# Kernel optimization log

Hardware: AMD Instinct MI355X
Metric: run time of the kernel (lower is better)

## Reference

```python
import jax, jax.numpy as jnp
import numpy as np

# ---- config (mirrors conf dict passed to RegionLoss.__init__) ----
ANCHORS = jnp.array([[1.3221, 1.73145], [3.19275, 4.00944], [5.05587, 8.09892],
                     [9.47112, 4.84053], [11.2364, 10.0071]], dtype=jnp.float32)
NUM_CLASSES = 80
OBJECT_SCALE = 5.0
NO_OBJECT_SCALE = 1.0
CLASS_SCALE = 1.0
COORD_SCALE = 1.0
SIL_THRESH = 0.6
SEEN = 0  # fresh module -> seen < 12800 warm-start branch is active


def _iou_center(a, b):
    """IoU of center-format boxes (cx, cy, w, h); a, b broadcastable [..., 4]."""
    ax1, ax2 = a[..., 0] - a[..., 2] * 0.5, a[..., 0] + a[..., 2] * 0.5
    ay1, ay2 = a[..., 1] - a[..., 3] * 0.5, a[..., 1] + a[..., 3] * 0.5
    bx1, bx2 = b[..., 0] - b[..., 2] * 0.5, b[..., 0] + b[..., 2] * 0.5
    by1, by2 = b[..., 1] - b[..., 3] * 0.5, b[..., 1] + b[..., 3] * 0.5
    iw = jnp.maximum(jnp.minimum(ax2, bx2) - jnp.maximum(ax1, bx1), 0.0)
    ih = jnp.maximum(jnp.minimum(ay2, by2) - jnp.maximum(ay1, by1), 0.0)
    inter = iw * ih
    union = a[..., 2] * a[..., 3] + b[..., 2] * b[..., 3] - inter
    return inter / union


def setup_inputs() -> dict:
    key = jax.random.key(0)
    k1, k2, k3, k4 = jax.random.split(key, 4)
    B, A, C, H, W, NBOX = 32, 5, NUM_CLASSES, 52, 52, 50
    pred = jax.random.normal(k1, (B, A * (C + 5), H, W), dtype=jnp.float32)
    cls = jax.random.randint(k2, (B, NBOX, 1), 0, C).astype(jnp.float32)
    xy = jax.random.uniform(k3, (B, NBOX, 2), minval=0.02, maxval=0.98, dtype=jnp.float32)
    wh = jax.random.uniform(k4, (B, NBOX, 2), minval=0.05, maxval=0.4, dtype=jnp.float32)
    target = jnp.concatenate([cls, xy, wh], axis=-1)  # (B, NBOX, 5): cls,x,y,w,h in [0,1]
    return {"pred": pred, "target": target, "train_out": 0}


def _region_loss(pred, target):
    B, H, W = pred.shape[0], pred.shape[2], pred.shape[3]
    A, C = ANCHORS.shape[0], NUM_CLASSES
    nbox = target.shape[1]
    p = pred.reshape(B, A, C + 5, H, W)

    txy = jax.nn.sigmoid(p[:, :, 0:2])                 # (B,A,2,H,W)
    twh = p[:, :, 2:4]                                 # (B,A,2,H,W)
    pred_no_off = jnp.concatenate([txy, twh], axis=2)  # (B,A,4,H,W)
    pred_conf = jax.nn.sigmoid(p[:, :, 4])             # (B,A,H,W)
    cls_logits = p[:, :, 5:]                           # (B,A,C,H,W)

    # decode boxes to grid units (detached in the original)
    grid_x = jnp.arange(W, dtype=p.dtype)              # broadcasts along W (last dim)
    grid_y = jnp.arange(H, dtype=p.dtype)[:, None]     # broadcasts along H
    aw = ANCHORS[:, 0][None, :, None, None]
    ah = ANCHORS[:, 1][None, :, None, None]
    bx = txy[:, :, 0] + grid_x
    by = txy[:, :, 1] + grid_y
    bw = jnp.exp(twh[:, :, 0]) * aw
    bh = jnp.exp(twh[:, :, 1]) * ah
    pred_boxes = jax.lax.stop_gradient(jnp.stack([bx, by, bw, bh], axis=-1))  # (B,A,H,W,4)

    # ground truth in grid units
    scale = jnp.array([W, H, W, H], dtype=p.dtype)
    gt = target[:, :, 1:5] * scale                     # (B,nbox,4) center format
    valid = target[:, :, 1] > 0                        # sentinel: x == 0 terminates

    # conf mask: zero-out cells whose best IoU vs any GT exceeds sil_thresh
    pb_flat = pred_boxes.reshape(B, A * H * W, 4)
    ious = _iou_center(gt[:, :, None, :], pb_flat[:, None, :, :])  # (B,nbox,A*H*W)
    ious = jnp.where(valid[:, :, None], ious, 0.0)
    max_iou = jnp.max(ious, axis=1).reshape(B, A, H, W)
    conf_mask = jnp.where(max_iou > SIL_THRESH, 0.0, NO_OBJECT_SCALE)

    # best anchor per GT via width/height-only IoU (boxes at origin)
    gw, gh = gt[..., 2], gt[..., 3]
    inter = jnp.minimum(gw[..., None], ANCHORS[:, 0]) * jnp.minimum(gh[..., None], ANCHORS[:, 1])
    union = gw[..., None] * gh[..., None] + ANCHORS[:, 0] * ANCHORS[:, 1] - inter
    best_a = jnp.argmax(inter / union, axis=-1)        # (B,nbox)

    gi = jnp.clip(gt[..., 0].astype(jnp.int32), 0, W - 1)
    gj = jnp.clip(gt[..., 1].astype(jnp.int32), 0, H - 1)
    b_idx = jnp.broadcast_to(jnp.arange(B)[:, None], (B, nbox))
    bi = jnp.where(valid, b_idx, B)                    # invalid GTs -> OOB batch, dropped

    aw_b = ANCHORS[best_a, 0]
    ah_b = ANCHORS[best_a, 1]
    tx_t = gt[..., 0] - gi.astype(p.dtype)
    ty_t = gt[..., 1] - gj.astype(p.dtype)
    tw_t = jnp.log(gw / aw_b)
    th_t = jnp.log(gh / ah_b)

    pred_box_at = pred_boxes[b_idx, best_a, gj, gi]    # (B,nbox,4) decoded box at GT cell
    iou_gt = _iou_center(gt, pred_box_at)              # (B,nbox)

    # initialize targets/masks (seen < 12800 warm start)
    if SEEN < 12800:
        coord_mask = jnp.ones((B, A, H, W), dtype=p.dtype)
        target_box = jnp.zeros((B, A, 4, H, W), dtype=p.dtype).at[:, :, 0:2].set(0.5)
    else:
        coord_mask = jnp.zeros((B, A, H, W), dtype=p.dtype)
        target_box = jnp.zeros((B, A, 4, H, W), dtype=p.dtype)
    cls_mask = jnp.zeros((B, A, H, W), dtype=p.dtype)
    target_conf = jnp.zeros((B, A, H, W), dtype=p.dtype)
    target_cls = jnp.zeros((B, A, H, W), dtype=p.dtype)

    coord_mask = coord_mask.at[bi, best_a, gj, gi].set(1.0, mode='drop')
    cls_mask = cls_mask.at[bi, best_a, gj, gi].set(1.0, mode='drop')
    conf_mask = conf_mask.at[bi, best_a, gj, gi].set(OBJECT_SCALE, mode='drop')
    target_box = target_box.at[bi, best_a, 0, gj, gi].set(tx_t, mode='drop')
    target_box = target_box.at[bi, best_a, 1, gj, gi].set(ty_t, mode='drop')
    target_box = target_box.at[bi, best_a, 2, gj, gi].set(tw_t, mode='drop')
    target_box = target_box.at[bi, best_a, 3, gj, gi].set(th_t, mode='drop')
    target_conf = target_conf.at[bi, best_a, gj, gi].set(iou_gt, mode='drop')
    target_cls = target_cls.at[bi, best_a, gj, gi].set(target[:, :, 0], mode='drop')

    # losses
    half = jnp.asarray(0.5, p.dtype)
    loss_x = COORD_SCALE * jnp.sum(((pred_no_off[:, :, 0] - target_box[:, :, 0]) * coord_mask) ** 2) * half
    loss_y = COORD_SCALE * jnp.sum(((pred_no_off[:, :, 1] - target_box[:, :, 1]) * coord_mask) ** 2) * half
    loss_w = COORD_SCALE * jnp.sum(((pred_no_off[:, :, 2] - target_box[:, :, 2]) * coord_mask) ** 2) * half
    loss_h = COORD_SCALE * jnp.sum(((pred_no_off[:, :, 3] - target_box[:, :, 3]) * coord_mask) ** 2) * half
    loss_conf = jnp.sum(((pred_conf - target_conf) * jnp.sqrt(conf_mask)) ** 2) * half

    logp = jax.nn.log_softmax(cls_logits, axis=2)      # (B,A,C,H,W)
    tcls = jnp.clip(target_cls.astype(jnp.int32), 0, C - 1)
    ce = -jnp.take_along_axis(logp, tcls[:, :, None], axis=2)[:, :, 0]  # (B,A,H,W)
    loss_cls = CLASS_SCALE * jnp.sum(cls_mask * ce)

    loss = loss_x + loss_y + loss_w + loss_h + loss_conf + loss_cls
    return loss, loss_x, loss_y, loss_w, loss_h, loss_conf, loss_cls


def reference(pred, target, train_out):
    out = _region_loss(pred, target)
    if train_out:
        return out
    return out[0]
```

## Files before the change

### kernel.cpp

```cpp
#include <hip/hip_runtime.h>
#include <math.h>

#define BB 32
#define AA 5
#define CC 80
#define HH 52
#define WW 52
#define NBOX 50
#define HWSZ (HH*WW)
#define CELLS (AA*HWSZ)

__constant__ float d_aw[AA] = {1.3221f, 3.19275f, 5.05587f, 9.47112f, 11.2364f};
__constant__ float d_ah[AA] = {1.73145f, 4.00944f, 8.09892f, 4.84053f, 10.0071f};

__device__ __forceinline__ float sig(float x) { return 1.f / (1.f + expf(-x)); }

__device__ __forceinline__ float wave_max(float v) {
    #pragma unroll
    for (int off = 32; off > 0; off >>= 1) v = fmaxf(v, __shfl_xor(v, off, 64));
    return v;
}
__device__ __forceinline__ float wave_sum(float v) {
    #pragma unroll
    for (int off = 32; off > 0; off >>= 1) v += __shfl_xor(v, off, 64);
    return v;
}

__global__ __launch_bounds__(256) void region_fused(const float* __restrict__ pred,
                                                    const float* __restrict__ target,
                                                    float* __restrict__ out) {
    __shared__ float4 s_box[NBOX];
    __shared__ float2 s_ac[NBOX];
    __shared__ float4 s_t[NBOX];
    __shared__ float2 s_m[NBOX];
    __shared__ float wsum[4];

    const int b = blockIdx.y;
    const int tid = threadIdx.x;
    const int lane = tid & 63;

    if (tid < NBOX) {
        const float* t = target + ((size_t)b * NBOX + tid) * 5;
        float t0 = t[0], t1 = t[1], t2 = t[2], t3 = t[3], t4 = t[4];
        float gx = t1 * (float)WW, gy = t2 * (float)HH;
        float gw = t3 * (float)WW, gh = t4 * (float)HH;
        bool valid = t1 > 0.f;
        int best = 0; float bestv = -1.f;
        #pragma unroll
        for (int a = 0; a < AA; ++a) {
            float inter = fminf(gw, d_aw[a]) * fminf(gh, d_ah[a]);
            float uni = gw * gh + d_aw[a] * d_ah[a] - inter;
            float r = inter / uni;
            if (r > bestv) { bestv = r; best = a; }
        }
        int gi = (int)gx; gi = gi < 0 ? 0 : (gi > WW - 1 ? WW - 1 : gi);
        int gj = (int)gy; gj = gj < 0 ? 0 : (gj > HH - 1 ? HH - 1 : gj);

        size_t bbase = ((size_t)(b * AA + best) * (CC + 5)) * HWSZ + (size_t)gj * WW + gi;
        float px = sig(pred[bbase]) + (float)gi;
        float py = sig(pred[bbase + HWSZ]) + (float)gj;
        float pw = expf(pred[bbase + 2 * HWSZ]) * d_aw[best];
        float ph = expf(pred[bbase + 3 * HWSZ]) * d_ah[best];

        float ax1 = gx - gw * 0.5f, ax2 = gx + gw * 0.5f;
        float ay1 = gy - gh * 0.5f, ay2 = gy + gh * 0.5f;
        float bx1 = px - pw * 0.5f, bx2 = px + pw * 0.5f;
        float by1 = py - ph * 0.5f, by2 = py + ph * 0.5f;
        float iw = fmaxf(fminf(ax2, bx2) - fmaxf(ax1, bx1), 0.f);
        float ih = fmaxf(fminf(ay2, by2) - fmaxf(ay1, by1), 0.f);
        float inter = iw * ih;
        float iou_gt = inter / (gw * gh + pw * ph - inter);

        if (valid) {
            s_box[tid] = make_float4(ax1, ax2, ay1, ay2);
            s_ac[tid]  = make_float2(0.375f * gw * gh,
                                     (float)(best * HWSZ + gj * WW + gi));
        } else {
            s_box[tid] = make_float4(0.f, 0.f, 0.f, 0.f);
            s_ac[tid]  = make_float2(0.f, -1.f);
        }
        s_t[tid] = make_float4(gx - (float)gi, gy - (float)gj,
                               logf(gw / d_aw[best]), logf(gh / d_ah[best]));
        s_m[tid] = make_float2(iou_gt, t0);
    }
    __syncthreads();

    const int c = blockIdx.x * 256 + tid;
    float lsum = 0.f;
    int win = -1;
    int a = 0, rem = 0, tcls = 0;
    if (c < CELLS) {
        a = c / HWSZ;
        rem = c - a * HWSZ;
        int hh = rem / WW;
        int wwi = rem - hh * WW;
        size_t base = ((size_t)(b * AA + a) * (CC + 5)) * HWSZ + rem;
        float p0 = pred[base];
        float p1 = pred[base + HWSZ];
        float p2 = pred[base + 2 * HWSZ];
        float p3 = pred[base + 3 * HWSZ];
        float p4 = pred[base + 4 * HWSZ];
        float tx = sig(p0);
        float ty = sig(p1);
        float conf = sig(p4);
        float bx = tx + (float)wwi;
        float by = ty + (float)hh;
        float bw = expf(p2) * d_aw[a];
        float bh = expf(p3) * d_ah[a];
        float px1 = bx - bw * 0.5f, px2 = bx + bw * 0.5f;
        float py1 = by - bh * 0.5f, py2 = by + bh * 0.5f;
        float tp = 0.375f * (bw * bh);
        float cf = (float)c;

        bool hit = false;
        #pragma unroll 5
        for (int j = 0; j < NBOX; ++j) {
            float4 r0 = s_box[j];
            float2 r1 = s_ac[j];
            float iw2 = fmaxf(fminf(px2, r0.y) - fmaxf(px1, r0.x), 0.f);
            float ih2 = fmaxf(fminf(py2, r0.w) - fmaxf(py1, r0.z), 0.f);
            float inter2 = iw2 * ih2;
            hit = hit | ((inter2 - tp) > r1.x);
            win = (r1.y == cf) ? j : win;
        }

        float dx, dy, dw, dh, lconf;
        if (win >= 0) {
            float4 r2 = s_t[win];
            float2 r3 = s_m[win];
            dx = tx - r2.x; dy = ty - r2.y; dw = p2 - r2.z; dh = p3 - r2.w;
            float d = conf - r3.x;
            lconf = 2.5f * d * d;
            int tc = (int)r3.y;
            tcls = tc < 0 ? 0 : (tc > CC - 1 ? CC - 1 : tc);
        } else {
            dx = tx - 0.5f; dy = ty - 0.5f; dw = p2; dh = p3;
            lconf = hit ? 0.f : 0.5f * conf * conf;
        }
        lsum = 0.5f * (dx * dx + dy * dy + dw * dw + dh * dh) + lconf;
    }

    unsigned long long mask = __ballot(win >= 0);
    while (mask) {
        int src = __ffsll(mask) - 1;
        mask &= mask - 1;
        int wa   = __shfl(a, src, 64);
        int wrem = __shfl(rem, src, 64);
        int wt   = __shfl(tcls, src, 64);
        size_t cbase = ((size_t)(b * AA + wa) * (CC + 5) + 5) * HWSZ + (size_t)wrem;
        float v1 = pred[cbase + (size_t)lane * HWSZ];
        float v2 = (lane < CC - 64) ? pred[cbase + (size_t)(lane + 64) * HWSZ]
                                    : -INFINITY;
        float mx = wave_max(fmaxf(v1, v2));
        float s = expf(v1 - mx) + ((lane < CC - 64) ? expf(v2 - mx) : 0.f);
        s = wave_sum(s);
        float vt = ((lane == wt) ? v1 : 0.f) + ((lane + 64 == wt) ? v2 : 0.f);
        vt = wave_sum(vt);
        if (lane == src) lsum += (mx + logf(s)) - vt;
    }

    #pragma unroll
    for (int off = 32; off > 0; off >>= 1)
        lsum += __shfl_down(lsum, off, 64);
    int wave = tid >> 6;
    if (lane == 0) wsum[wave] = lsum;
    __syncthreads();
    if (tid == 0) {
        atomicAdd(out, wsum[0] + wsum[1] + wsum[2] + wsum[3]);
    }
}

extern "C" void kernel_launch(void* const* d_in, const int* in_sizes, int n_in,
                              void* d_out, int out_size, void* d_ws, size_t ws_size,
                              hipStream_t stream) {
    const float* pred = (const float*)d_in[0];
    const float* target = (const float*)d_in[1];
    float* out = (float*)d_out;

    hipMemsetAsync(out, 0, sizeof(float) * out_size, stream);
    dim3 grid((CELLS + 255) / 256, BB);
    region_fused<<<grid, dim3(256), 0, stream>>>(pred, target, out);
}
```

Before: 204.7 us.

## Process four cells per thread to amortize per-block target setup and shared loads

Each thread now handles four grid cells strided by 16 blocks, and the grid shrinks from 53 to 16 blocks per batch image. The per-block target preprocessing and each shared-memory box read are reused across four cells in the inner IoU loop. This trades lower block count, and so less parallelism (512 blocks total), for less redundant setup work and more memory loads in flight per thread.

```diff
diff --git a/kernel.cpp b/kernel.cpp
--- a/kernel.cpp
+++ b/kernel.cpp
@@ -9,6 +9,8 @@
 #define NBOX 50
 #define HWSZ (HH*WW)
 #define CELLS (AA*HWSZ)
+#define NCH 4
+#define CSTRIDE (16*256)
 
 __constant__ float d_aw[AA] = {1.3221f, 3.19275f, 5.05587f, 9.47112f, 11.2364f};
 __constant__ float d_ah[AA] = {1.73145f, 4.00944f, 8.09892f, 4.84053f, 10.0071f};
@@ -85,21 +87,37 @@
     }
     __syncthreads();
 
-    const int c = blockIdx.x * 256 + tid;
+    const int c0 = blockIdx.x * 256 + tid;
+
+    float px1[NCH], px2[NCH], py1[NCH], py2[NCH], tp[NCH], cf[NCH];
+    float p2s[NCH], p3s[NCH], txs[NCH], tys[NCH], cfs[NCH];
+    int aA[NCH], remA[NCH], win[NCH], tcl[NCH];
+    bool hit[NCH], act[NCH];
+
     float lsum = 0.f;
-    int win = -1;
-    int a = 0, rem = 0, tcls = 0;
-    if (c < CELLS) {
-        a = c / HWSZ;
-        rem = c - a * HWSZ;
+
+    #pragma unroll
+    for (int k = 0; k < NCH; ++k) {
+        int c = c0 + k * CSTRIDE;
+        act[k] = (c < CELLS);
+        win[k] = -1;
+        hit[k] = false;
+        tcl[k] = 0;
+        int cc = act[k] ? c : 0;
+        int a = cc / HWSZ;
+        int rem = cc - a * HWSZ;
+        aA[k] = a; remA[k] = rem;
         int hh = rem / WW;
         int wwi = rem - hh * WW;
-        size_t base = ((size_t)(b * AA + a) * (CC + 5)) * HWSZ + rem;
-        float p0 = pred[base];
-        float p1 = pred[base + HWSZ];
-        float p2 = pred[base + 2 * HWSZ];
-        float p3 = pred[base + 3 * HWSZ];
-        float p4 = pred[base + 4 * HWSZ];
+        float p0 = 0.f, p1 = 0.f, p2 = 0.f, p3 = 0.f, p4 = 0.f;
+        if (act[k]) {
+            size_t base = ((size_t)(b * AA + a) * (CC + 5)) * HWSZ + rem;
+            p0 = pred[base];
+            p1 = pred[base + HWSZ];
+            p2 = pred[base + 2 * HWSZ];
+            p3 = pred[base + 3 * HWSZ];
+            p4 = pred[base + 4 * HWSZ];
+        }
         float tx = sig(p0);
         float ty = sig(p1);
         float conf = sig(p4);
@@ -107,56 +125,67 @@
         float by = ty + (float)hh;
         float bw = expf(p2) * d_aw[a];
         float bh = expf(p3) * d_ah[a];
-        float px1 = bx - bw * 0.5f, px2 = bx + bw * 0.5f;
-        float py1 = by - bh * 0.5f, py2 = by + bh * 0.5f;
-        float tp = 0.375f * (bw * bh);
-        float cf = (float)c;
-
-        bool hit = false;
-        #pragma unroll 5
-        for (int j = 0; j < NBOX; ++j) {
-            float4 r0 = s_box[j];
-            float2 r1 = s_ac[j];
-            float iw2 = fmaxf(fminf(px2, r0.y) - fmaxf(px1, r0.x), 0.f);
-            float ih2 = fmaxf(fminf(py2, r0.w) - fmaxf(py1, r0.z), 0.f);
+        px1[k] = bx - bw * 0.5f; px2[k] = bx + bw * 0.5f;
+        py1[k] = by - bh * 0.5f; py2[k] = by + bh * 0.5f;
+        tp[k] = 0.375f * (bw * bh);
+        cf[k] = act[k] ? (float)c : -2.f;
+        p2s[k] = p2; p3s[k] = p3; txs[k] = tx; tys[k] = ty; cfs[k] = conf;
+    }
+
+    #pragma unroll 2
+    for (int j = 0; j < NBOX; ++j) {
+        float4 r0 = s_box[j];
+        float2 r1 = s_ac[j];
+        #pragma unroll
+        for (int k = 0; k < NCH; ++k) {
+            float iw2 = fmaxf(fminf(px2[k], r0.y) - fmaxf(px1[k], r0.x), 0.f);
+            float ih2 = fmaxf(fminf(py2[k], r0.w) - fmaxf(py1[k], r0.z), 0.f);
             float inter2 = iw2 * ih2;
-            hit = hit | ((inter2 - tp) > r1.x);
-            win = (r1.y == cf) ? j : win;
-        }
-
+            hit[k] = hit[k] | ((inter2 - tp[k]) > r1.x);
+            win[k] = (r1.y == cf[k]) ? j : win[k];
+        }
+    }
+
+    #pragma unroll
+    for (int k = 0; k < NCH; ++k) {
+        if (!act[k]) continue;
+        float tx = txs[k], ty = tys[k], p2 = p2s[k], p3 = p3s[k], conf = cfs[k];
         float dx, dy, dw, dh, lconf;
-        if (win >= 0) {
-            float4 r2 = s_t[win];
-            float2 r3 = s_m[win];
+        if (win[k] >= 0) {
+            float4 r2 = s_t[win[k]];
+            float2 r3 = s_m[win[k]];
             dx = tx - r2.x; dy = ty - r2.y; dw = p2 - r2.z; dh = p3 - r2.w;
             float d = conf - r3.x;
             lconf = 2.5f * d * d;
             int tc = (int)r3.y;
-            tcls = tc < 0 ? 0 : (tc > CC - 1 ? CC - 1 : tc);
+            tcl[k] = tc < 0 ? 0 : (tc > CC - 1 ? CC - 1 : tc);
         } else {
             dx = tx - 0.5f; dy = ty - 0.5f; dw = p2; dh = p3;
-            lconf = hit ? 0.f : 0.5f * conf * conf;
-        }
-        lsum = 0.5f * (dx * dx + dy * dy + dw * dw + dh * dh) + lconf;
-    }
-
-    unsigned long long mask = __ballot(win >= 0);
-    while (mask) {
-        int src = __ffsll(mask) - 1;
-        mask &= mask - 1;
-        int wa   = __shfl(a, src, 64);
-        int wrem = __shfl(rem, src, 64);
-        int wt   = __shfl(tcls, src, 64);
-        size_t cbase = ((size_t)(b * AA + wa) * (CC + 5) + 5) * HWSZ + (size_t)wrem;
-        float v1 = pred[cbase + (size_t)lane * HWSZ];
-        float v2 = (lane < CC - 64) ? pred[cbase + (size_t)(lane + 64) * HWSZ]
-                                    : -INFINITY;
-        float mx = wave_max(fmaxf(v1, v2));
-        float s = expf(v1 - mx) + ((lane < CC - 64) ? expf(v2 - mx) : 0.f);
-        s = wave_sum(s);
-        float vt = ((lane == wt) ? v1 : 0.f) + ((lane + 64 == wt) ? v2 : 0.f);
-        vt = wave_sum(vt);
-        if (lane == src) lsum += (mx + logf(s)) - vt;
+            lconf = hit[k] ? 0.f : 0.5f * conf * conf;
+        }
+        lsum += 0.5f * (dx * dx + dy * dy + dw * dw + dh * dh) + lconf;
+    }
+
+    #pragma unroll
+    for (int k = 0; k < NCH; ++k) {
+        unsigned long long mask = __ballot(win[k] >= 0);
+        while (mask) {
+            int src = __ffsll(mask) - 1;
+            mask &= mask - 1;
+            int wa   = __shfl(aA[k], src, 64);
+            int wrem = __shfl(remA[k], src, 64);
+            int wt   = __shfl(tcl[k], src, 64);
+            size_t cbase = ((size_t)(b * AA + wa) * (CC + 5) + 5) * HWSZ + (size_t)wrem;
+            float v1 = pred[cbase + (size_t)lane * HWSZ];
+            float v2 = (lane < CC - 64) ? pred[cbase + (size_t)(lane + 64) * HWSZ]
+                                        : -INFINITY;
+            float mx = wave_max(fmaxf(v1, v2));
+            float s = expf(v1 - mx) + ((lane < CC - 64) ? expf(v2 - mx) : 0.f);
+            s = wave_sum(s);
+            float vt = ((lane == wt) ? v1 : 0.f) + ((lane + 64 == wt) ? v2 : 0.f);
+            vt = wave_sum(vt);
+            if (lane == src) lsum += (mx + logf(s)) - vt;
+        }
     }
 
     #pragma unroll
@@ -178,6 +207,6 @@
     float* out = (float*)d_out;
 
     hipMemsetAsync(out, 0, sizeof(float) * out_size, stream);
-    dim3 grid((CELLS + 255) / 256, BB);
+    dim3 grid(16, BB);
     region_fused<<<grid, dim3(256), 0, stream>>>(pred, target, out);
 }
```

After: 203.3 us. About the same (-0.7%).
